# Kernel optimization log

Hardware: AMD Instinct MI355X
Metric: run time of the kernel (lower is better)

## Reference

```python
import jax, jax.numpy as jnp
import numpy as np

HIDDEN = 128
N_RBF = 32
LMAX = 2
N_NODES = 10000
DEG = 8  # each node has DEG outgoing (and DEG incoming) edges on a ring


def _build_graph():
    src = np.repeat(np.arange(N_NODES, dtype=np.int64), DEG)
    offs = np.tile(np.arange(1, DEG + 1, dtype=np.int64), N_NODES)
    dst = (src + offs) % N_NODES
    keys = src * N_NODES + dst
    order = np.argsort(keys)
    src2, dst2 = src[order], dst[order]  # e2 sorted by key (searchsorted invariant)
    e1_to_e2 = np.empty_like(order)
    e1_to_e2[order] = np.arange(order.size)
    return src, dst, src2, dst2, e1_to_e2


def setup_inputs() -> dict:
    key = jax.random.key(0)
    ks = jax.random.split(key, 12)
    src1, dst1, src2, dst2, e1_to_e2 = _build_graph()
    E1, E2 = src1.size, src2.size
    in_dim = 6 * HIDDEN + 3 * N_RBF + 1  # 865

    def lin(k, fi, fo):
        kw, kb = jax.random.split(k)
        s = 1.0 / np.sqrt(fi)
        return (jax.random.uniform(kw, (fi, fo), minval=-s, maxval=s),
                jax.random.uniform(kb, (fo,), minval=-s, maxval=s))

    w1, b1 = lin(ks[0], in_dim, HIDDEN)
    w2, b2 = lin(ks[1], HIDDEN, HIDDEN)
    wgw, bgw = lin(ks[2], HIDDEN, HIDDEN)
    wgt, bgt = lin(ks[3], HIDDEN, HIDDEN)
    return {
        "t_e2": jax.random.normal(ks[4], (E2, HIDDEN), dtype=jnp.float32),
        "h": jax.random.normal(ks[5], (N_NODES, HIDDEN), dtype=jnp.float32),
        "edge_index1": jnp.asarray(np.stack([src1, dst1])),
        "edge_index2": jnp.asarray(np.stack([src2, dst2])),
        "e1_to_e2": jnp.asarray(e1_to_e2),
        "dist_e1": jax.random.uniform(ks[6], (E1,), dtype=jnp.float32),
        "dist_e2": jax.random.uniform(ks[7], (E2,), dtype=jnp.float32),
        "rbf_e1": jax.random.normal(ks[8], (E1, N_RBF), dtype=jnp.float32),
        "rbf_e2": jax.random.normal(ks[9], (E2, N_RBF), dtype=jnp.float32),
        "sph_e1": jax.random.normal(ks[10], (E1, LMAX + 1), dtype=jnp.float32),
        "num_nodes": N_NODES,
        "w1": w1, "b1": b1, "w2": w2, "b2": b2,
        "wgw": wgw, "bgw": bgw, "wgt": wgt, "bgt": bgt,
    }


def _wedge_indices(edge_index1, edge_index2, num_nodes):
    """Host-side (numpy, vectorized) wedge construction: for every center node k,
    all (incoming edge i->k, outgoing edge k->j) pairs with i != j, kept only when
    (i, j) itself is an edge in e2 (looked up by sorted key search)."""
    src1 = np.asarray(edge_index1[0]); dst1 = np.asarray(edge_index1[1])
    src2 = np.asarray(edge_index2[0]); dst2 = np.asarray(edge_index2[1])
    nz = src1 != dst1  # drop self-loops
    s, d = src1[nz], dst1[nz]
    eid = np.nonzero(nz)[0]
    out_deg = np.bincount(s, minlength=num_nodes)
    out_order = np.argsort(s, kind="stable")  # filtered-edge positions grouped by src
    out_ptr = np.concatenate([np.zeros(1, np.int64), np.cumsum(out_deg)])
    reps = out_deg[d]  # each incoming edge pairs with out_deg[center] outgoing edges
    total = int(reps.sum())
    if total == 0:
        z = np.zeros(0, np.int64)
        return z, z, z, z, z, z
    starts = np.cumsum(reps) - reps
    local = np.arange(total) - np.repeat(starts, reps)
    kj_f = out_order[np.repeat(out_ptr[d], reps) + local]
    i = np.repeat(s, reps)
    k = np.repeat(d, reps)
    eik = np.repeat(eid, reps)
    j = d[kj_f]
    ekj = eid[kj_f]
    m = i != j
    i, k, j, eik, ekj = i[m], k[m], j[m], eik[m], ekj[m]
    e2_keys = src2.astype(np.int64) * num_nodes + dst2
    pk = i.astype(np.int64) * num_nodes + j
    pos = np.searchsorted(e2_keys, pk)
    posc = np.minimum(pos, e2_keys.size - 1)
    valid = (pos < e2_keys.size) & (e2_keys[posc] == pk)
    return i[valid], k[valid], j[valid], eik[valid], ekj[valid], posc[valid]


def reference(t_e2, h, edge_index1, edge_index2, e1_to_e2, dist_e1, dist_e2,
              rbf_e1, rbf_e2, sph_e1, num_nodes,
              w1, b1, w2, b2, wgw, bgw, wgt, bgt):
    i, k, j, eik, ekj, eij = _wedge_indices(edge_index1, edge_index2, int(num_nodes))
    if i.size == 0:
        return t_e2
    i, k, j = jnp.asarray(i), jnp.asarray(k), jnp.asarray(j)
    eik, ekj, eij = jnp.asarray(eik), jnp.asarray(ekj), jnp.asarray(eij)
    e1e2 = jnp.asarray(e1_to_e2)
    # wedge geometric features (wedge_use_high_degree=False -> l=1 contraction only)
    c_feat = (sph_e1[eik, 1] * sph_e1[ekj, 1])[:, None]           # [W, 1]
    g = jnp.concatenate([rbf_e1[eik], rbf_e1[ekj], rbf_e2[eij], c_feat], axis=-1)
    rho_in = jnp.concatenate([t_e2[e1e2[eik]], t_e2[e1e2[ekj]], t_e2[eij],
                              h[i], h[k], h[j], g], axis=-1)       # [W, 865]
    msg = jax.nn.silu(rho_in @ w1 + b1) @ w2 + b2                  # [W, H]
    m = jax.ops.segment_sum(msg, eij, num_segments=t_e2.shape[0])  # [E2, H]
    return t_e2 + jax.nn.sigmoid(m @ wgw + bgw) * jnp.tanh(t_e2 @ wgt + bgt)
```

## Files before the change

kernel.cpp:

```cpp
#include <hip/hip_runtime.h>
#include <math.h>

typedef unsigned short u16;
typedef unsigned int u32;
typedef __bf16 bf16x8 __attribute__((ext_vector_type(8)));
typedef float f32x4 __attribute__((ext_vector_type(4)));

__device__ __forceinline__ float bf2f(u16 v){ union{u32 u;float f;}c; c.u=((u32)v)<<16; return c.f; }
__device__ __forceinline__ u16 f2bf(float f){ union{float f;u32 u;}c; c.f=f; u32 l=(c.u>>16)&1u; c.u+=0x7fffu+l; return (u16)(c.u>>16); }
__device__ __forceinline__ u32 pk2(float a, float b){ return (u32)f2bf(a) | ((u32)f2bf(b)<<16); }
__device__ __forceinline__ uint4 ld8f(const float* p){
  float4 x = ((const float4*)p)[0];
  float4 y = ((const float4*)p)[1];
  uint4 r; r.x=pk2(x.x,x.y); r.y=pk2(x.z,x.w); r.z=pk2(y.x,y.y); r.w=pk2(y.z,y.w);
  return r;
}
__device__ __forceinline__ float fsilu(float x){ return x/(1.f+__expf(-x)); }


__global__ void k_setup_edges(const int* __restrict__ e1_to_e2,
                              const float* __restrict__ rbf_e1,
                              const float* __restrict__ sph_e1,
                              u16* __restrict__ rbf1p,
                              float* __restrict__ sph_c, int E1) {
  int e = blockIdx.x*256 + threadIdx.x;
  if (e >= E1) return;
  int f = e1_to_e2[e];
  sph_c[f] = sph_e1[e*3+1];
  const float* s = rbf_e1 + (size_t)e*32;
  uint4* d = (uint4*)(rbf1p + (size_t)f*32);
  d[0]=ld8f(s); d[1]=ld8f(s+8); d[2]=ld8f(s+16); d[3]=ld8f(s+24);
}

__global__ void k_out_ptr(const int* __restrict__ src2, int* __restrict__ out_ptr,
                          int Nn, int E2) {
  int n = blockIdx.x*256 + threadIdx.x;
  if (n > Nn) return;
  int lo=0, hi=E2;
  while (lo<hi){ int m=(lo+hi)>>1; if (src2[m]<n) lo=m+1; else hi=m; }
  out_ptr[n]=lo;
}

__global__ void k_wbigt(const float* __restrict__ w1, u16* __restrict__ WbigT) {
  int id = blockIdx.x*256+threadIdx.x;
  if (id >= 384*448) return;
  int n = id/448, k = id%448;
  int q = n>>7, nn = n&127;
  int row = -1;
  if (k<128) row = q*128+k;
  else if (k<256) { if (q==0) row = 384+(k-128); }
  else if (k<384) { if (q==0) row = 512+(k-256); else if (q==1) row = 640+(k-256); }
  else if (k<416) { if (q==0) row = 768+(k-384); else if (q==1) row = 800+(k-384); }
  else { if (q==2) row = 832+(k-416); }
  WbigT[id] = (row>=0) ? f2bf(w1[row*128+nn]) : (u16)0;
}

__global__ void k_smallw(const float* __restrict__ w2, const float* __restrict__ wgw,
                         const float* __restrict__ wgt, const float* __restrict__ b2,
                         u16* __restrict__ WcT, u16* __restrict__ WgtT,
                         float* __restrict__ bc2) {
  int id = blockIdx.x*256+threadIdx.x;
  if (id < 16384) {
    int n = id&127, k = id>>7;
    float s = 0.f;
    for (int r=0;r<128;r++) s += w2[k*128+r]*wgw[r*128+n];
    WcT[n*128+k] = f2bf(s);
    WgtT[n*128+k] = f2bf(wgt[k*128+n]);
  } else if (id < 16384+128) {
    int n = id-16384;
    float s = 0.f;
    for (int r=0;r<128;r++) s += b2[r]*wgw[r*128+n];
    bc2[n] = s;
  }
}

__global__ __launch_bounds__(256, 8)
void k_enum(const int* __restrict__ src2, const int* __restrict__ dst2,
            const int* __restrict__ out_ptr, const float* __restrict__ sph_c,
            int4* __restrict__ wrec, int* __restrict__ cnt, int E2) {
  int id = blockIdx.x*256 + threadIdx.x;
  if (id >= E2*8) return;
  int gw = id >> 3, d = id & 7;
  int i = src2[gw], j = dst2[gw];
  int f = out_ptr[i] + d;
  if (f >= out_ptr[i+1]) return;
  int k = dst2[f];
  int lo = out_ptr[k], hi = out_ptr[k+1], hi0 = hi;
  while (lo<hi) { int m=(lo+hi)>>1; if (dst2[m]<j) lo=m+1; else hi=m; }
  if (lo < hi0 && dst2[lo]==j) {
    float cf = sph_c[f]*sph_c[lo];
    int slot = atomicAdd(&cnt[gw], 1);
    int4 r; r.x=f; r.y=lo; r.z=__float_as_int(cf); r.w=0;
    wrec[(size_t)gw*8 + slot] = r;
  }
}

__global__ __launch_bounds__(256, 8)
void k_wedge2(const u16* __restrict__ Q1, const u16* __restrict__ Q2,
              const u16* __restrict__ P3, const int4* __restrict__ wrec,
              const int* __restrict__ cnt, const float* __restrict__ w1,
              u16* __restrict__ S, int E2) {
  int gw = (int)((blockIdx.x*256 + threadIdx.x) >> 6);
  int lane = threadIdx.x & 63;
  if (gw >= E2) return;
  u32 p3u = ((const u32*)(P3 + (size_t)gw*128))[lane];
  float p30 = bf2f((u16)(p3u&0xffff)), p31 = bf2f((u16)(p3u>>16));
  float2 wv = ((const float2*)(w1 + 864*128))[lane];
  const u32* q1b = (const u32*)Q1;
  const u32* q2b = (const u32*)Q2;
  const int4* wr = wrec + (size_t)gw*8;
  int c = cnt[gw];
  float a0=0.f, a1=0.f;
  int w = 0;
  for (; w+2<=c; w+=2) {
    int4 rA = wr[w], rB = wr[w+1];
    u32 xA = q1b[(size_t)rA.x*64 + lane];
    u32 yA = q2b[(size_t)rA.y*64 + lane];
    u32 xB = q1b[(size_t)rB.x*64 + lane];
    u32 yB = q2b[(size_t)rB.y*64 + lane];
    float cfA = __int_as_float(rA.z), cfB = __int_as_float(rB.z);
    float x0 = p30 + bf2f((u16)(xA&0xffff)) + bf2f((u16)(yA&0xffff)) + cfA*wv.x;
    float x1 = p31 + bf2f((u16)(xA>>16))    + bf2f((u16)(yA>>16))    + cfA*wv.y;
    float z0 = p30 + bf2f((u16)(xB&0xffff)) + bf2f((u16)(yB&0xffff)) + cfB*wv.x;
    float z1 = p31 + bf2f((u16)(xB>>16))    + bf2f((u16)(yB>>16))    + cfB*wv.y;
    a0 += fsilu(x0) + fsilu(z0);
    a1 += fsilu(x1) + fsilu(z1);
  }
  if (w < c) {
    int4 rA = wr[w];
    u32 xA = q1b[(size_t)rA.x*64 + lane];
    u32 yA = q2b[(size_t)rA.y*64 + lane];
    float cfA = __int_as_float(rA.z);
    float x0 = p30 + bf2f((u16)(xA&0xffff)) + bf2f((u16)(yA&0xffff)) + cfA*wv.x;
    float x1 = p31 + bf2f((u16)(xA>>16))    + bf2f((u16)(yA>>16))    + cfA*wv.y;
    a0 += fsilu(x0);
    a1 += fsilu(x1);
  }
  ((u32*)(S + (size_t)gw*128))[lane] = pk2(a0, a1);
}

struct GArgs {
  const float* t_f32; const float* h; const float* rbf_e2;
  const u16* rbf1p; const u16* Asrc;
  const int* src2; const int* dst2; const int* cnt;
  const u16* Bmat; const u16* Gin;
  const float* b1; const float* bgw; const float* bgt; const float* bc2;
  u16* out0; u16* out1; u16* out2;
  float* outf;
  int M;
};

template<int MODE>
__global__ __launch_bounds__(256, 2)
void k_gemm(GArgs a) {
  constexpr int KT = (MODE==0)?448:128;
  constexpr int NK = KT/32;
  __shared__ u16 As[128*40];
  __shared__ u16 Bs[128*40];
  const int tid = threadIdx.x;
  const int bm = blockIdx.x, bn = blockIdx.y;
  const int lane = tid & 63, wave = tid >> 6;
  const int wm = wave >> 1, wn = wave & 1;
  const int quad = lane >> 4, l16 = lane & 15;

  const int part = tid & 3;
  const int ra = tid >> 2;
  const int rb = ra + 64;
  long fa = (long)bm*128 + ra;
  long fb = (long)bm*128 + rb;
  if (fa >= a.M) fa = a.M-1;
  if (fb >= a.M) fb = a.M-1;
  int sa=0, da=0, sb=0, db=0;
  if constexpr (MODE==0) { sa=a.src2[fa]; da=a.dst2[fa]; sb=a.src2[fb]; db=a.dst2[fb]; }

  f32x4 acc[4][4] = {};
  for (int ks=0; ks<NK; ks++) {
    const int kb = ks*32;
    uint4 va, vb;
    if constexpr (MODE==0) {
      if (ks<4)       { va = ld8f(a.t_f32 + fa*128 + kb + part*8);
                        vb = ld8f(a.t_f32 + fb*128 + kb + part*8); }
      else if (ks<8)  { va = ld8f(a.h + (long)sa*128 + (kb-128) + part*8);
                        vb = ld8f(a.h + (long)sb*128 + (kb-128) + part*8); }
      else if (ks<12) { va = ld8f(a.h + (long)da*128 + (kb-256) + part*8);
                        vb = ld8f(a.h + (long)db*128 + (kb-256) + part*8); }
      else if (ks==12){ va = *(const uint4*)(a.rbf1p + fa*32 + part*8);
                        vb = *(const uint4*)(a.rbf1p + fb*32 + part*8); }
      else            { va = ld8f(a.rbf_e2 + fa*32 + part*8);
                        vb = ld8f(a.rbf_e2 + fb*32 + part*8); }
    } else if constexpr (MODE==1) {
      va = *(const uint4*)(a.Asrc + fa*128 + kb + part*8);
      vb = *(const uint4*)(a.Asrc + fb*128 + kb + part*8);
    } else {
      va = ld8f(a.t_f32 + fa*128 + kb + part*8);
      vb = ld8f(a.t_f32 + fb*128 + kb + part*8);
    }
    uint4 wa = *(const uint4*)(a.Bmat + (long)(bn*128 + ra)*KT + kb + part*8);
    uint4 wb = *(const uint4*)(a.Bmat + (long)(bn*128 + rb)*KT + kb + part*8);
    __syncthreads();
    *(uint4*)(As + ra*40 + part*8) = va;
    *(uint4*)(As + rb*40 + part*8) = vb;
    *(uint4*)(Bs + ra*40 + part*8) = wa;
    *(uint4*)(Bs + rb*40 + part*8) = wb;
    __syncthreads();
    bf16x8 af[4], bfr[4];
    #pragma unroll
    for (int t=0;t<4;t++) {
      af[t]  = *(const bf16x8*)(As + (wm*64 + t*16 + l16)*40 + quad*8);
      bfr[t] = *(const bf16x8*)(Bs + (wn*64 + t*16 + l16)*40 + quad*8);
    }
    #pragma unroll
    for (int tm=0;tm<4;tm++)
      #pragma unroll
      for (int tn=0;tn<4;tn++)
        acc[tm][tn] = __builtin_amdgcn_mfma_f32_16x16x32_bf16(af[tm], bfr[tn], acc[tm][tn], 0,0,0);
  }

  #pragma unroll
  for (int tm=0;tm<4;tm++) {
    const int rloc = wm*64 + tm*16 + quad*4;
    #pragma unroll
    for (int r=0;r<4;r++) {
      long row = (long)bm*128 + rloc + r;
      if (row >= a.M) continue;
      #pragma unroll
      for (int tn=0;tn<4;tn++) {
        const int col = wn*64 + tn*16 + l16;
        float v = acc[tm][tn][r];
        if constexpr (MODE==0) {
          u16* dst = (bn==0)? a.out0 : (bn==1)? a.out1 : a.out2;
          if (bn==2) v += a.b1[col];
          dst[row*128 + col] = f2bf(v);
        } else if constexpr (MODE==1) {
          float u = v + (float)a.cnt[row]*a.bc2[col] + a.bgw[col];
          float g = 1.f/(1.f+__expf(-u));
          a.out0[row*128+col] = f2bf(g);
        } else {
          float vv = v + a.bgt[col];
          float th = 1.f - 2.f/(__expf(2.f*vv)+1.f);
          float t  = a.t_f32[row*128+col];
          float g  = bf2f(a.Gin[row*128+col]);
          a.outf[row*128+col] = t + g*th;
        }
      }
    }
  }
}

extern "C" void kernel_launch(void* const* d_in, const int* in_sizes, int n_in,
                              void* d_out, int out_size, void* d_ws, size_t ws_size,
                              hipStream_t stream) {
  const float* t_e2  = (const float*)d_in[0];
  const float* h     = (const float*)d_in[1];
  const int* ei2     = (const int*)d_in[3];
  const int* e1_to_e2 = (const int*)d_in[4];
  const float* rbf_e1 = (const float*)d_in[7];
  const float* rbf_e2 = (const float*)d_in[8];
  const float* sph_e1 = (const float*)d_in[9];
  const float* w1  = (const float*)d_in[11];
  const float* b1  = (const float*)d_in[12];
  const float* w2  = (const float*)d_in[13];
  const float* b2  = (const float*)d_in[14];
  const float* wgw = (const float*)d_in[15];
  const float* bgw = (const float*)d_in[16];
  const float* wgt = (const float*)d_in[17];
  const float* bgt = (const float*)d_in[18];

  const int E2 = in_sizes[0]/128;
  const int Nn = in_sizes[1]/128;
  const int E1 = in_sizes[5];
  const int* src2 = ei2;
  const int* dst2 = ei2 + E2;

  char* p = (char*)d_ws;
  u16* Q1 = (u16*)p;       p += (size_t)E2*128*2;
  u16* Q2 = (u16*)p;       p += (size_t)E2*128*2;
  u16* P3 = (u16*)p;       p += (size_t)E2*128*2;
  u16* rbf1p = (u16*)p;    p += (size_t)E2*32*2;
  u16* WbigT = (u16*)p;    p += (size_t)384*448*2;
  u16* WcT   = (u16*)p;    p += (size_t)128*128*2;
  u16* WgtT  = (u16*)p;    p += (size_t)128*128*2;
  float* sph_c = (float*)p; p += (size_t)E2*4;
  float* bc2   = (float*)p; p += 512;
  int* out_ptr = (int*)p;   p += (((size_t)(Nn+1)*4 + 63)/64)*64;
  int* cnt     = (int*)p;   p += (size_t)E2*4;
  int4* wrec   = (int4*)p;  p += (size_t)E2*8*16;
  u16* S = P3;
  u16* G = Q1;

  hipMemsetAsync(cnt, 0, (size_t)E2*4, stream);

  k_setup_edges<<<(E1+255)/256, 256, 0, stream>>>(e1_to_e2, rbf_e1, sph_e1, rbf1p, sph_c, E1);
  k_out_ptr<<<(Nn+1+255)/256, 256, 0, stream>>>(src2, out_ptr, Nn, E2);
  k_wbigt<<<(384*448+255)/256, 256, 0, stream>>>(w1, WbigT);
  k_smallw<<<(16512+255)/256, 256, 0, stream>>>(w2, wgw, wgt, b2, WcT, WgtT, bc2);
  k_enum<<<(E2*8+255)/256, 256, 0, stream>>>(src2, dst2, out_ptr, sph_c, wrec, cnt, E2);

  const int Mb = (E2+127)/128;
  {
    GArgs a = {};
    a.t_f32=t_e2; a.h=h; a.rbf1p=rbf1p; a.rbf_e2=rbf_e2;
    a.src2=src2; a.dst2=dst2; a.Bmat=WbigT; a.b1=b1;
    a.out0=Q1; a.out1=Q2; a.out2=P3; a.M=E2;
    k_gemm<0><<<dim3(Mb,3), 256, 0, stream>>>(a);
  }
  k_wedge2<<<(E2+3)/4, 256, 0, stream>>>(Q1, Q2, P3, wrec, cnt, w1, S, E2);
  {
    GArgs a = {};
    a.Asrc=S; a.cnt=cnt; a.Bmat=WcT; a.bgw=bgw; a.bc2=bc2;
    a.out0=G; a.M=E2;
    k_gemm<1><<<dim3(Mb,1), 256, 0, stream>>>(a);
  }
  {
    GArgs a = {};
    a.t_f32=t_e2; a.Bmat=WgtT; a.bgt=bgt; a.Gin=G;
    a.outf=(float*)d_out; a.M=E2;
    k_gemm<2><<<dim3(Mb,1), 256, 0, stream>>>(a);
  }
}
```

Measured before the change: 337.4 us.

## Fuse setup kernels, merge final two GEMMs, remap GEMM0 blocks per XCD

Four setup kernels and the cnt memset are merged into one launch that dispatches on block-index ranges. The gate GEMM and the tanh GEMM are fused into one kernel with two accumulator sets, which removes the bf16 G intermediate round-trip and one launch. GEMM0 becomes a 1D grid whose block ids are remapped so that consecutive tiles land on the same XCD, aiming for better L2 reuse of the shared A rows. The bf16 conversion now uses the native __bf16 cast, and the doubled accumulators raise register pressure in the fused GEMM.

```diff
diff --git a/kernel.cpp b/kernel.cpp
--- a/kernel.cpp
+++ b/kernel.cpp
@@ -7,8 +7,10 @@
 typedef float f32x4 __attribute__((ext_vector_type(4)));
 
 __device__ __forceinline__ float bf2f(u16 v){ union{u32 u;float f;}c; c.u=((u32)v)<<16; return c.f; }
-__device__ __forceinline__ u16 f2bf(float f){ union{float f;u32 u;}c; c.f=f; u32 l=(c.u>>16)&1u; c.u+=0x7fffu+l; return (u16)(c.u>>16); }
-__device__ __forceinline__ u32 pk2(float a, float b){ return (u32)f2bf(a) | ((u32)f2bf(b)<<16); }
+__device__ __forceinline__ u16 f2bf(float f){ union{__bf16 h; u16 u;}c; c.h=(__bf16)f; return c.u; }
+__device__ __forceinline__ u32 pk2(float a, float b){
+  union{ __bf16 h[2]; u32 u; }c; c.h[0]=(__bf16)a; c.h[1]=(__bf16)b; return c.u;
+}
 __device__ __forceinline__ uint4 ld8f(const float* p){
   float4 x = ((const float4*)p)[0];
   float4 y = ((const float4*)p)[1];
@@ -17,60 +19,62 @@
 }
 __device__ __forceinline__ float fsilu(float x){ return x/(1.f+__expf(-x)); }
 
-
-__global__ void k_setup_edges(const int* __restrict__ e1_to_e2,
-                              const float* __restrict__ rbf_e1,
-                              const float* __restrict__ sph_e1,
-                              u16* __restrict__ rbf1p,
-                              float* __restrict__ sph_c, int E1) {
-  int e = blockIdx.x*256 + threadIdx.x;
-  if (e >= E1) return;
-  int f = e1_to_e2[e];
-  sph_c[f] = sph_e1[e*3+1];
-  const float* s = rbf_e1 + (size_t)e*32;
-  uint4* d = (uint4*)(rbf1p + (size_t)f*32);
-  d[0]=ld8f(s); d[1]=ld8f(s+8); d[2]=ld8f(s+16); d[3]=ld8f(s+24);
-}
-
-__global__ void k_out_ptr(const int* __restrict__ src2, int* __restrict__ out_ptr,
-                          int Nn, int E2) {
-  int n = blockIdx.x*256 + threadIdx.x;
-  if (n > Nn) return;
-  int lo=0, hi=E2;
-  while (lo<hi){ int m=(lo+hi)>>1; if (src2[m]<n) lo=m+1; else hi=m; }
-  out_ptr[n]=lo;
-}
-
-__global__ void k_wbigt(const float* __restrict__ w1, u16* __restrict__ WbigT) {
-  int id = blockIdx.x*256+threadIdx.x;
-  if (id >= 384*448) return;
-  int n = id/448, k = id%448;
-  int q = n>>7, nn = n&127;
-  int row = -1;
-  if (k<128) row = q*128+k;
-  else if (k<256) { if (q==0) row = 384+(k-128); }
-  else if (k<384) { if (q==0) row = 512+(k-256); else if (q==1) row = 640+(k-256); }
-  else if (k<416) { if (q==0) row = 768+(k-384); else if (q==1) row = 800+(k-384); }
-  else { if (q==2) row = 832+(k-416); }
-  WbigT[id] = (row>=0) ? f2bf(w1[row*128+nn]) : (u16)0;
-}
-
-__global__ void k_smallw(const float* __restrict__ w2, const float* __restrict__ wgw,
-                         const float* __restrict__ wgt, const float* __restrict__ b2,
-                         u16* __restrict__ WcT, u16* __restrict__ WgtT,
-                         float* __restrict__ bc2) {
-  int id = blockIdx.x*256+threadIdx.x;
-  if (id < 16384) {
-    int n = id&127, k = id>>7;
-    float s = 0.f;
-    for (int r=0;r<128;r++) s += w2[k*128+r]*wgw[r*128+n];
-    WcT[n*128+k] = f2bf(s);
-    WgtT[n*128+k] = f2bf(wgt[k*128+n]);
-  } else if (id < 16384+128) {
-    int n = id-16384;
-    float s = 0.f;
-    for (int r=0;r<128;r++) s += b2[r]*wgw[r*128+n];
-    bc2[n] = s;
+__global__ void k_setup_all(const int* __restrict__ e1_to_e2,
+                            const float* __restrict__ rbf_e1,
+                            const float* __restrict__ sph_e1,
+                            u16* __restrict__ rbf1p, float* __restrict__ sph_c, int E1,
+                            const int* __restrict__ src2, int* __restrict__ out_ptr,
+                            int Nn, int E2,
+                            const float* __restrict__ w1, u16* __restrict__ WbigT,
+                            const float* __restrict__ w2, const float* __restrict__ wgw,
+                            const float* __restrict__ wgt, const float* __restrict__ b2,
+                            u16* __restrict__ WcT, u16* __restrict__ WgtT,
+                            float* __restrict__ bc2, int* __restrict__ cnt,
+                            int nb0, int nb1, int nb2, int nb3) {
+  const int b = blockIdx.x, t = threadIdx.x;
+  if (b < nb0) {
+    int e = b*256 + t;
+    if (e >= E1) return;
+    int f = e1_to_e2[e];
+    sph_c[f] = sph_e1[e*3+1];
+    const float* s = rbf_e1 + (size_t)e*32;
+    uint4* d = (uint4*)(rbf1p + (size_t)f*32);
+    d[0]=ld8f(s); d[1]=ld8f(s+8); d[2]=ld8f(s+16); d[3]=ld8f(s+24);
+  } else if (b < nb1) {
+    int n = (b-nb0)*256 + t;
+    if (n > Nn) return;
+    int lo=0, hi=E2;
+    while (lo<hi){ int m=(lo+hi)>>1; if (src2[m]<n) lo=m+1; else hi=m; }
+    out_ptr[n]=lo;
+  } else if (b < nb2) {
+    int id = (b-nb1)*256 + t;
+    if (id >= 384*448) return;
+    int n = id/448, k = id%448;
+    int q = n>>7, nn = n&127;
+    int row = -1;
+    if (k<128) row = q*128+k;
+    else if (k<256) { if (q==0) row = 384+(k-128); }
+    else if (k<384) { if (q==0) row = 512+(k-256); else if (q==1) row = 640+(k-256); }
+    else if (k<416) { if (q==0) row = 768+(k-384); else if (q==1) row = 800+(k-384); }
+    else { if (q==2) row = 832+(k-416); }
+    WbigT[id] = (row>=0) ? f2bf(w1[row*128+nn]) : (u16)0;
+  } else if (b < nb3) {
+    int id = (b-nb2)*256 + t;
+    if (id < 16384) {
+      int n = id&127, k = id>>7;
+      float s = 0.f;
+      for (int r=0;r<128;r++) s += w2[k*128+r]*wgw[r*128+n];
+      WcT[n*128+k] = f2bf(s);
+      WgtT[n*128+k] = f2bf(wgt[k*128+n]);
+    } else if (id < 16384+128) {
+      int n = id-16384;
+      float s = 0.f;
+      for (int r=0;r<128;r++) s += b2[r]*wgw[r*128+n];
+      bc2[n] = s;
+    }
+  } else {
+    int i = (b-nb3)*256 + t;
+    if (i < E2) cnt[i] = 0;
   }
 }
 
@@ -143,22 +147,27 @@
   const float* t_f32; const float* h; const float* rbf_e2;
   const u16* rbf1p; const u16* Asrc;
   const int* src2; const int* dst2; const int* cnt;
-  const u16* Bmat; const u16* Gin;
+  const u16* Bmat; const u16* Bmat2;
   const float* b1; const float* bgw; const float* bgt; const float* bc2;
   u16* out0; u16* out1; u16* out2;
   float* outf;
   int M;
 };
 
-template<int MODE>
 __global__ __launch_bounds__(256, 2)
-void k_gemm(GArgs a) {
-  constexpr int KT = (MODE==0)?448:128;
+void k_gemm0(GArgs a) {
+  const int nwg = gridDim.x;
+  const int id  = blockIdx.x;
+  const int xcd = id & 7, idx = id >> 3;
+  const int q = nwg >> 3, r = nwg & 7;
+  const int w = (xcd < r ? xcd*(q+1) : r*(q+1) + (xcd-r)*q) + idx;
+  const int bm = w/3, bn = w - bm*3;
+
+  constexpr int KT = 448;
   constexpr int NK = KT/32;
   __shared__ u16 As[128*40];
   __shared__ u16 Bs[128*40];
   const int tid = threadIdx.x;
-  const int bm = blockIdx.x, bn = blockIdx.y;
   const int lane = tid & 63, wave = tid >> 6;
   const int wm = wave >> 1, wn = wave & 1;
   const int quad = lane >> 4, l16 = lane & 15;
@@ -170,31 +179,22 @@
   long fb = (long)bm*128 + rb;
   if (fa >= a.M) fa = a.M-1;
   if (fb >= a.M) fb = a.M-1;
-  int sa=0, da=0, sb=0, db=0;
-  if constexpr (MODE==0) { sa=a.src2[fa]; da=a.dst2[fa]; sb=a.src2[fb]; db=a.dst2[fb]; }
+  const int sa=a.src2[fa], da=a.dst2[fa], sb=a.src2[fb], db=a.dst2[fb];
 
   f32x4 acc[4][4] = {};
   for (int ks=0; ks<NK; ks++) {
     const int kb = ks*32;
     uint4 va, vb;
-    if constexpr (MODE==0) {
-      if (ks<4)       { va = ld8f(a.t_f32 + fa*128 + kb + part*8);
-                        vb = ld8f(a.t_f32 + fb*128 + kb + part*8); }
-      else if (ks<8)  { va = ld8f(a.h + (long)sa*128 + (kb-128) + part*8);
-                        vb = ld8f(a.h + (long)sb*128 + (kb-128) + part*8); }
-      else if (ks<12) { va = ld8f(a.h + (long)da*128 + (kb-256) + part*8);
-                        vb = ld8f(a.h + (long)db*128 + (kb-256) + part*8); }
-      else if (ks==12){ va = *(const uint4*)(a.rbf1p + fa*32 + part*8);
-                        vb = *(const uint4*)(a.rbf1p + fb*32 + part*8); }
-      else            { va = ld8f(a.rbf_e2 + fa*32 + part*8);
-                        vb = ld8f(a.rbf_e2 + fb*32 + part*8); }
-    } else if constexpr (MODE==1) {
-      va = *(const uint4*)(a.Asrc + fa*128 + kb + part*8);
-      vb = *(const uint4*)(a.Asrc + fb*128 + kb + part*8);
-    } else {
-      va = ld8f(a.t_f32 + fa*128 + kb + part*8);
-      vb = ld8f(a.t_f32 + fb*128 + kb + part*8);
-    }
+    if (ks<4)       { va = ld8f(a.t_f32 + fa*128 + kb + part*8);
+                      vb = ld8f(a.t_f32 + fb*128 + kb + part*8); }
+    else if (ks<8)  { va = ld8f(a.h + (long)sa*128 + (kb-128) + part*8);
+                      vb = ld8f(a.h + (long)sb*128 + (kb-128) + part*8); }
+    else if (ks<12) { va = ld8f(a.h + (long)da*128 + (kb-256) + part*8);
+                      vb = ld8f(a.h + (long)db*128 + (kb-256) + part*8); }
+    else if (ks==12){ va = *(const uint4*)(a.rbf1p + fa*32 + part*8);
+                      vb = *(const uint4*)(a.rbf1p + fb*32 + part*8); }
+    else            { va = ld8f(a.rbf_e2 + fa*32 + part*8);
+                      vb = ld8f(a.rbf_e2 + fb*32 + part*8); }
     uint4 wa = *(const uint4*)(a.Bmat + (long)(bn*128 + ra)*KT + kb + part*8);
     uint4 wb = *(const uint4*)(a.Bmat + (long)(bn*128 + rb)*KT + kb + part*8);
     __syncthreads();
@@ -227,21 +227,99 @@
       for (int tn=0;tn<4;tn++) {
         const int col = wn*64 + tn*16 + l16;
         float v = acc[tm][tn][r];
-        if constexpr (MODE==0) {
-          u16* dst = (bn==0)? a.out0 : (bn==1)? a.out1 : a.out2;
-          if (bn==2) v += a.b1[col];
-          dst[row*128 + col] = f2bf(v);
-        } else if constexpr (MODE==1) {
-          float u = v + (float)a.cnt[row]*a.bc2[col] + a.bgw[col];
-          float g = 1.f/(1.f+__expf(-u));
-          a.out0[row*128+col] = f2bf(g);
-        } else {
-          float vv = v + a.bgt[col];
-          float th = 1.f - 2.f/(__expf(2.f*vv)+1.f);
-          float t  = a.t_f32[row*128+col];
-          float g  = bf2f(a.Gin[row*128+col]);
-          a.outf[row*128+col] = t + g*th;
-        }
+        u16* dst = (bn==0)? a.out0 : (bn==1)? a.out1 : a.out2;
+        if (bn==2) v += a.b1[col];
+        dst[row*128 + col] = f2bf(v);
+      }
+    }
+  }
+}
+
+__global__ __launch_bounds__(256, 2)
+void k_gemm12(GArgs a) {
+  __shared__ u16 As[128*40];
+  __shared__ u16 Bs[128*40];
+  const int tid = threadIdx.x;
+  const int bm = blockIdx.x;
+  const int lane = tid & 63, wave = tid >> 6;
+  const int wm = wave >> 1, wn = wave & 1;
+  const int quad = lane >> 4, l16 = lane & 15;
+
+  const int part = tid & 3;
+  const int ra = tid >> 2;
+  const int rb = ra + 64;
+  long fa = (long)bm*128 + ra;
+  long fb = (long)bm*128 + rb;
+  if (fa >= a.M) fa = a.M-1;
+  if (fb >= a.M) fb = a.M-1;
+
+  f32x4 acc1[4][4] = {};
+  f32x4 acc2[4][4] = {};
+  for (int ks=0; ks<4; ks++) {
+    const int kb = ks*32;
+    uint4 va = *(const uint4*)(a.Asrc + fa*128 + kb + part*8);
+    uint4 vb = *(const uint4*)(a.Asrc + fb*128 + kb + part*8);
+    uint4 wa = *(const uint4*)(a.Bmat + (long)ra*128 + kb + part*8);
+    uint4 wbv= *(const uint4*)(a.Bmat + (long)rb*128 + kb + part*8);
+    __syncthreads();
+    *(uint4*)(As + ra*40 + part*8) = va;
+    *(uint4*)(As + rb*40 + part*8) = vb;
+    *(uint4*)(Bs + ra*40 + part*8) = wa;
+    *(uint4*)(Bs + rb*40 + part*8) = wbv;
+    __syncthreads();
+    bf16x8 af[4], bfr[4];
+    #pragma unroll
+    for (int t=0;t<4;t++) {
+      af[t]  = *(const bf16x8*)(As + (wm*64 + t*16 + l16)*40 + quad*8);
+      bfr[t] = *(const bf16x8*)(Bs + (wn*64 + t*16 + l16)*40 + quad*8);
+    }
+    #pragma unroll
+    for (int tm=0;tm<4;tm++)
+      #pragma unroll
+      for (int tn=0;tn<4;tn++)
+        acc1[tm][tn] = __builtin_amdgcn_mfma_f32_16x16x32_bf16(af[tm], bfr[tn], acc1[tm][tn], 0,0,0);
+  }
+  for (int ks=0; ks<4; ks++) {
+    const int kb = ks*32;
+    uint4 va = ld8f(a.t_f32 + fa*128 + kb + part*8);
+    uint4 vb = ld8f(a.t_f32 + fb*128 + kb + part*8);
+    uint4 wa = *(const uint4*)(a.Bmat2 + (long)ra*128 + kb + part*8);
+    uint4 wbv= *(const uint4*)(a.Bmat2 + (long)rb*128 + kb + part*8);
+    __syncthreads();
+    *(uint4*)(As + ra*40 + part*8) = va;
+    *(uint4*)(As + rb*40 + part*8) = vb;
+    *(uint4*)(Bs + ra*40 + part*8) = wa;
+    *(uint4*)(Bs + rb*40 + part*8) = wbv;
+    __syncthreads();
+    bf16x8 af[4], bfr[4];
+    #pragma unroll
+    for (int t=0;t<4;t++) {
+      af[t]  = *(const bf16x8*)(As + (wm*64 + t*16 + l16)*40 + quad*8);
+      bfr[t] = *(const bf16x8*)(Bs + (wn*64 + t*16 + l16)*40 + quad*8);
+    }
+    #pragma unroll
+    for (int tm=0;tm<4;tm++)
+      #pragma unroll
+      for (int tn=0;tn<4;tn++)
+        acc2[tm][tn] = __builtin_amdgcn_mfma_f32_16x16x32_bf16(af[tm], bfr[tn], acc2[tm][tn], 0,0,0);
+  }
+
+  #pragma unroll
+  for (int tm=0;tm<4;tm++) {
+    const int rloc = wm*64 + tm*16 + quad*4;
+    #pragma unroll
+    for (int r=0;r<4;r++) {
+      long row = (long)bm*128 + rloc + r;
+      if (row >= a.M) continue;
+      #pragma unroll
+      for (int tn=0;tn<4;tn++) {
+        const int col = wn*64 + tn*16 + l16;
+        float u = acc1[tm][tn][r] + (float)a.cnt[row]*a.bc2[col] + a.bgw[col];
+        float g = 1.f/(1.f+__expf(-u));
+        float vv = acc2[tm][tn][r] + a.bgt[col];
+        float th = 1.f - 2.f/(__expf(2.f*vv)+1.f);
+        float t  = a.t_f32[row*128+col];
+        a.outf[row*128+col] = t + g*th;
       }
     }
   }
@@ -286,14 +364,22 @@
   int* cnt     = (int*)p;   p += (size_t)E2*4;
   int4* wrec   = (int4*)p;  p += (size_t)E2*8*16;
   u16* S = P3;
-  u16* G = Q1;
-
-  hipMemsetAsync(cnt, 0, (size_t)E2*4, stream);
-
-  k_setup_edges<<<(E1+255)/256, 256, 0, stream>>>(e1_to_e2, rbf_e1, sph_e1, rbf1p, sph_c, E1);
-  k_out_ptr<<<(Nn+1+255)/256, 256, 0, stream>>>(src2, out_ptr, Nn, E2);
-  k_wbigt<<<(384*448+255)/256, 256, 0, stream>>>(w1, WbigT);
-  k_smallw<<<(16512+255)/256, 256, 0, stream>>>(w2, wgw, wgt, b2, WcT, WgtT, bc2);
+
+  const int nb_edges = (E1+255)/256;
+  const int nb_ptr   = (Nn+1+255)/256;
+  const int nb_wbig  = (384*448+255)/256;
+  const int nb_small = (16512+255)/256;
+  const int nb_cnt   = (E2+255)/256;
+  const int nb0 = nb_edges;
+  const int nb1 = nb0 + nb_ptr;
+  const int nb2 = nb1 + nb_wbig;
+  const int nb3 = nb2 + nb_small;
+  const int nbT = nb3 + nb_cnt;
+  k_setup_all<<<nbT, 256, 0, stream>>>(e1_to_e2, rbf_e1, sph_e1, rbf1p, sph_c, E1,
+                                       src2, out_ptr, Nn, E2,
+                                       w1, WbigT, w2, wgw, wgt, b2,
+                                       WcT, WgtT, bc2, cnt,
+                                       nb0, nb1, nb2, nb3);
   k_enum<<<(E2*8+255)/256, 256, 0, stream>>>(src2, dst2, out_ptr, sph_c, wrec, cnt, E2);
 
   const int Mb = (E2+127)/128;
@@ -302,19 +388,14 @@
     a.t_f32=t_e2; a.h=h; a.rbf1p=rbf1p; a.rbf_e2=rbf_e2;
     a.src2=src2; a.dst2=dst2; a.Bmat=WbigT; a.b1=b1;
     a.out0=Q1; a.out1=Q2; a.out2=P3; a.M=E2;
-    k_gemm<0><<<dim3(Mb,3), 256, 0, stream>>>(a);
+    k_gemm0<<<Mb*3, 256, 0, stream>>>(a);
   }
   k_wedge2<<<(E2+3)/4, 256, 0, stream>>>(Q1, Q2, P3, wrec, cnt, w1, S, E2);
   {
     GArgs a = {};
-    a.Asrc=S; a.cnt=cnt; a.Bmat=WcT; a.bgw=bgw; a.bc2=bc2;
-    a.out0=G; a.M=E2;
-    k_gemm<1><<<dim3(Mb,1), 256, 0, stream>>>(a);
-  }
-  {
-    GArgs a = {};
-    a.t_f32=t_e2; a.Bmat=WgtT; a.bgt=bgt; a.Gin=G;
+    a.Asrc=S; a.cnt=cnt; a.Bmat=WcT; a.Bmat2=WgtT;
+    a.bgw=bgw; a.bgt=bgt; a.bc2=bc2; a.t_f32=t_e2;
     a.outf=(float*)d_out; a.M=E2;
-    k_gemm<2><<<dim3(Mb,1), 256, 0, stream>>>(a);
-  }
-}
+    k_gemm12<<<Mb, 256, 0, stream>>>(a);
+  }
+}
```

Measured after the change: 329.5 us. -2.3%, faster.
